# Kernel optimization log

Measured on AMD Instinct MI355X. Metric: run time of the kernel, lower is better.

Reference implementation:

```python
import jax, jax.numpy as jnp
import numpy as np

B, S, D, H = 1, 2048, 1024, 16
HD = D // H  # head_dim = 64
ROPE_BASE = 10000.0


def _rope_cos_sin(seqlen, head_dim, dtype):
    inv_freq = 1.0 / (ROPE_BASE ** (jnp.arange(0, head_dim, 2, dtype=jnp.float32) / head_dim))
    t = jnp.arange(seqlen, dtype=jnp.float32)
    freqs = jnp.outer(t, inv_freq)                      # [S, HD/2]
    emb = jnp.concatenate([freqs, freqs], axis=-1)      # [S, HD]
    # broadcast shape [1, S, 1, HD] over (batch, seq, heads, head_dim)
    return jnp.cos(emb)[None, :, None, :].astype(dtype), jnp.sin(emb)[None, :, None, :].astype(dtype)


def _rotate_half(x):
    x1, x2 = jnp.split(x, 2, axis=-1)
    return jnp.concatenate([-x2, x1], axis=-1)


def setup_inputs() -> dict:
    key = jax.random.key(0)
    k1, k2, k3 = jax.random.split(key, 3)
    std_in = 1.0 / np.sqrt(D)
    std_out = std_in / np.sqrt(2.0)  # layer_id = 0
    x = jax.random.normal(k1, (B, S, D), dtype=jnp.float32)
    w_in = jax.random.normal(k2, (3 * H * HD, D), dtype=jnp.float32) * std_in
    w_out = jax.random.normal(k3, (D, H * HD), dtype=jnp.float32) * std_out
    return {"x": x, "w_in": w_in, "w_out": w_out, "is_causal": 1}


def reference(x, w_in, w_out, is_causal):
    b, s, _ = x.shape
    qkv = jnp.einsum('bsd,ed->bse', x, w_in)            # [B,S,3*H*HD]
    xq, xk, xv = jnp.split(qkv, 3, axis=-1)
    xq = xq.reshape(b, s, H, HD)
    xk = xk.reshape(b, s, H, HD)
    xv = xv.reshape(b, s, H, HD)
    cos, sin = _rope_cos_sin(s, HD, xq.dtype)
    xq = xq * cos + _rotate_half(xq) * sin
    xk = xk * cos + _rotate_half(xk) * sin
    scale = 1.0 / np.sqrt(HD)
    scores = jnp.einsum('bqhd,bkhd->bhqk', xq, xk) * scale  # [B,H,S,S]
    if is_causal:
        mask = jnp.tril(jnp.ones((s, s), dtype=bool))
        scores = jnp.where(mask[None, None], scores, jnp.finfo(scores.dtype).min)
    probs = jax.nn.softmax(scores, axis=-1)
    out = jnp.einsum('bhqk,bkhd->bqhd', probs, xv)      # [B,S,H,HD]
    out = out.reshape(b, s, H * HD)
    return jnp.einsum('bse,de->bsd', out, w_out)
```

## Files before the change

### kernel.cpp

```cpp
#include <hip/hip_runtime.h>
#include <stdint.h>

#define S_LEN 2048
#define DMODEL 1024
#define NHEAD 16
#define HDIM 64
#define NE 3072
#define C2 0.18033688011112042f
#define RINV (-13.287712379549449f / 32.f)

typedef __attribute__((ext_vector_type(8))) short short8_t;
typedef __attribute__((ext_vector_type(4))) float f32x4;
typedef __attribute__((ext_vector_type(16))) float f32x16;

__device__ __forceinline__ float bf2f(ushort u) {
  union { float f; uint32_t i; } c; c.i = ((uint32_t)u) << 16; return c.f;
}
__device__ __forceinline__ ushort f2bf(float f) {
  union { float f; uint32_t i; } c; c.f = f;
  uint32_t x = c.i;
  return (ushort)((x + 0x7fffu + ((x >> 16) & 1u)) >> 16);
}

__device__ __forceinline__ void gload_lds16(const ushort* g, ushort* l) {
  __builtin_amdgcn_global_load_lds(
      (const __attribute__((address_space(1))) void*)g,
      (__attribute__((address_space(3))) void*)l, 16, 0, 0);
}

__global__ void cvt_all(const float* __restrict__ x, const float* __restrict__ w_in,
                        const float* __restrict__ w_out,
                        ushort* __restrict__ xbf, ushort* __restrict__ winbf,
                        ushort* __restrict__ woutbf) {
  int i = blockIdx.x * blockDim.x + threadIdx.x;
  const float* src; ushort* dst; int off;
  if (i < 524288)       { src = x;     dst = xbf;    off = i; }
  else if (i < 1310720) { src = w_in;  dst = winbf;  off = i - 524288; }
  else                  { src = w_out; dst = woutbf; off = i - 1310720; }
  float4 v = ((const float4*)src)[off];
  ushort4 o;
  o.x = f2bf(v.x); o.y = f2bf(v.y); o.z = f2bf(v.z); o.w = f2bf(v.w);
  ((ushort4*)dst)[off] = o;
}

template<int BM, int BN, int OUT_BF16>
__global__ __launch_bounds__(256) void gemm_abt(
    const ushort* __restrict__ A, const ushort* __restrict__ B,
    void* __restrict__ Cv, int M, int N, int K)
{
  constexpr int AR = BM / 32;
  constexpr int AC = BN / 32;
  constexpr int PG = (BM + BN) / 32;
  __shared__ ushort lds[(BM + BN) * 64];

  const int nbn = N / BN;
  const int cpx = gridDim.x >> 3;
  const int bid = blockIdx.x;
  const int swz = (bid & 7) * cpx + (bid >> 3);
  const int bm = swz / nbn;
  const int bn = swz - bm * nbn;
  const int tid = threadIdx.x;
  const int w = tid >> 6, l = tid & 63;
  const int wm = w >> 1, wn = w & 1;
  const int fr = l & 15, fg = l >> 4;

  f32x4 acc[AR][AC];
#pragma unroll
  for (int r = 0; r < AR; ++r)
#pragma unroll
    for (int c = 0; c < AC; ++c) acc[r][c] = (f32x4){0.f, 0.f, 0.f, 0.f};

  const ushort* gsrc[PG];
  ushort* ldst[PG];
#pragma unroll
  for (int i = 0; i < PG; ++i) {
    int ch = w + 4 * i;
    int row = ch * 8 + (l >> 3);
    if (row < BM)
      gsrc[i] = A + (size_t)(bm * BM + row) * K + (l & 7) * 8;
    else
      gsrc[i] = B + (size_t)(bn * BN + (row - BM)) * K + (l & 7) * 8;
    ldst[i] = &lds[ch * 512];
  }

  const ushort* fa = &lds[(wm * (BM / 2) + fr) * 64 + fg * 8];
  const ushort* fb = &lds[BM * 64 + (wn * (BN / 2) + fr) * 64 + fg * 8];

  for (int k0 = 0; k0 < K; k0 += 64) {
    __syncthreads();
#pragma unroll
    for (int i = 0; i < PG; ++i) gload_lds16(gsrc[i] + k0, ldst[i]);
    __syncthreads();

    short8_t af[AR][2], bfr[AC][2];
#pragma unroll
    for (int r = 0; r < AR; ++r)
#pragma unroll
      for (int kk = 0; kk < 2; ++kk) {
        union { short8_t v; uint4 q; } u;
        u.q = *(const uint4*)(fa + r * 1024 + kk * 32);
        af[r][kk] = u.v;
      }
#pragma unroll
    for (int c = 0; c < AC; ++c)
#pragma unroll
      for (int kk = 0; kk < 2; ++kk) {
        union { short8_t v; uint4 q; } u;
        u.q = *(const uint4*)(fb + c * 1024 + kk * 32);
        bfr[c][kk] = u.v;
      }
    __builtin_amdgcn_s_setprio(1);
#pragma unroll
    for (int kk = 0; kk < 2; ++kk)
#pragma unroll
      for (int r = 0; r < AR; ++r)
#pragma unroll
        for (int c = 0; c < AC; ++c)
          acc[r][c] = __builtin_amdgcn_mfma_f32_16x16x32_bf16(af[r][kk], bfr[c][kk], acc[r][c], 0, 0, 0);
    __builtin_amdgcn_s_setprio(0);
  }

  const int row0 = bm * BM + wm * (BM / 2) + fg * 4;
  const int col0 = bn * BN + wn * (BN / 2) + fr;
#pragma unroll
  for (int r = 0; r < AR; ++r)
#pragma unroll
    for (int c = 0; c < AC; ++c)
#pragma unroll
      for (int j = 0; j < 4; ++j) {
        int row = row0 + r * 16 + j;
        int col = col0 + c * 16;
        if (OUT_BF16)
          ((ushort*)Cv)[(size_t)row * N + col] = f2bf(acc[r][c][j]);
        else
          ((float*)Cv)[(size_t)row * N + col] = acc[r][c][j];
      }
}

__global__ __launch_bounds__(256) void transform_kv(
    const ushort* __restrict__ qkv, ushort* __restrict__ kfrag, ushort* __restrict__ vfrag)
{
  __shared__ ushort Kt[64][72];
  __shared__ ushort Vt[64][72];
  const int h = blockIdx.x & 15, t = blockIdx.x >> 4;
  const int tid = threadIdx.x;
#pragma unroll
  for (int it = 0; it < 2; ++it) {
    int idx = tid + 256 * it;
    int key = idx >> 3, d8 = (idx & 7) << 3;
    const ushort* src = qkv + (size_t)(t * 64 + key) * NE + DMODEL + h * HDIM + d8;
    *(uint4*)&Kt[key][d8] = *(const uint4*)src;
    *(uint4*)&Vt[key][d8] = *(const uint4*)(src + DMODEL);
  }
  __syncthreads();

  {
    const int i = tid & 31;
    const int k8 = (tid >> 5) * 8;
    float invf = exp2f((float)i * RINV);
#pragma unroll
    for (int kk = 0; kk < 8; ++kk) {
      int key = k8 + kk;
      float sn, cs;
      sincosf((float)(t * 64 + key) * invf, &sn, &cs);
      float x1 = bf2f(Kt[key][i]), x2 = bf2f(Kt[key][i + 32]);
      Kt[key][i]      = f2bf(x1 * cs - x2 * sn);
      Kt[key][i + 32] = f2bf(x2 * cs + x1 * sn);
    }
  }
  __syncthreads();

  ushort* kb = kfrag + (size_t)(h * 32 + t) * 4096;
  ushort* vb = vfrag + (size_t)(h * 32 + t) * 4096;
#pragma unroll
  for (int it = 0; it < 2; ++it) {
    int idx = tid + 256 * it;
    int c = idx >> 6, l = idx & 63;
    int q = l & 31, hi = l >> 5;
    int kh = c >> 2, ks = c & 3;
    uint4 v = *(const uint4*)&Kt[32 * kh + q][16 * ks + 8 * hi];
    *(uint4*)(kb + idx * 8) = v;
  }
#pragma unroll
  for (int it = 0; it < 2; ++it) {
    int idx = tid + 256 * it;
    int c = idx >> 6, l = idx & 63;
    int q = l & 31, hi = l >> 5;
    int ks = c >> 1, dh = c & 1;
    ushort tmp[8];
#pragma unroll
    for (int jj = 0; jj < 8; ++jj)
      tmp[jj] = Vt[16 * ks + 8 * hi + jj][32 * dh + q];
    *(uint4*)(vb + idx * 8) = *(const uint4*)tmp;
  }
}

__global__ __launch_bounds__(256) void attn_mfma(
    const ushort* __restrict__ qkv, const ushort* __restrict__ kfrag,
    const ushort* __restrict__ vfrag, ushort* __restrict__ O,
    const int* __restrict__ icausal)
{
  __shared__ ushort obf[4][32][68];
  __shared__ float2 mdl[4][32];

  const int h = blockIdx.x & 15;
  const int i = blockIdx.x >> 4;
  const int g = i & 15, k = i >> 4;
  const int qt = (k == 0) ? g : (k == 1) ? (63 - g) : (k == 2) ? (31 - g) : (32 + g);

  const int causal = *icausal;
  const int nt = causal ? ((qt >> 1) + 1) : (S_LEN / 64);

  const int tid = threadIdx.x;
  const int w = tid >> 6, l = tid & 63;
  const int q = l & 31, hi = l >> 5;
  const int q0 = qt * 32;
  const int qa = q0 + q;
  const int t0 = w * nt / 4, t1 = (w + 1) * nt / 4;

  short8_t qf[4];
  {
    const ushort* qp = qkv + (size_t)qa * NE + h * HDIM + 8 * hi;
#pragma unroll
    for (int ks = 0; ks < 4; ++ks) {
      union { short8_t v; uint4 u; } uu;
      uu.u = *(const uint4*)(qp + 16 * ks);
      qf[ks] = uu.v;
    }
    union { short8_t v; ushort u[8]; } a0, a1, b0, b1;
    a0.v = qf[0]; a1.v = qf[1]; b0.v = qf[2]; b1.v = qf[3];
#pragma unroll
    for (int j = 0; j < 8; ++j) {
      {
        float invf = exp2f((float)(8 * hi + j) * RINV);
        float sn, cs; sincosf((float)qa * invf, &sn, &cs);
        float x1 = bf2f(a0.u[j]), x2 = bf2f(b0.u[j]);
        a0.u[j] = f2bf(x1 * cs - x2 * sn);
        b0.u[j] = f2bf(x2 * cs + x1 * sn);
      }
      {
        float invf = exp2f((float)(16 + 8 * hi + j) * RINV);
        float sn, cs; sincosf((float)qa * invf, &sn, &cs);
        float x1 = bf2f(a1.u[j]), x2 = bf2f(b1.u[j]);
        a1.u[j] = f2bf(x1 * cs - x2 * sn);
        b1.u[j] = f2bf(x2 * cs + x1 * sn);
      }
    }
    qf[0] = a0.v; qf[1] = a1.v; qf[2] = b0.v; qf[3] = b1.v;
  }

  const ushort* kb = kfrag + (size_t)(h * 32 + t0) * 4096 + l * 8;
  const ushort* vb = vfrag + (size_t)(h * 32 + t0) * 4096 + l * 8;

  float m_run = -1e30f, den = 0.f;
  f32x16 oacc[2];
#pragma unroll
  for (int d = 0; d < 2; ++d)
#pragma unroll
    for (int r = 0; r < 16; ++r) oacc[d][r] = 0.f;

  if (t0 < t1) {
    uint4 kq[8];
#pragma unroll
    for (int ks = 0; ks < 4; ++ks)
#pragma unroll
      for (int kh = 0; kh < 2; ++kh)
        kq[ks * 2 + kh] = *(const uint4*)(kb + (kh * 4 + ks) * 512);
    kb += 4096;

    for (int t = t0; t < t1; ++t) {
      uint4 vq[8];
#pragma unroll
      for (int c = 0; c < 8; ++c)
        vq[c] = *(const uint4*)(vb + c * 512);
      vb += 4096;

      f32x16 sacc[2];
#pragma unroll
      for (int kh = 0; kh < 2; ++kh)
#pragma unroll
        for (int r = 0; r < 16; ++r) sacc[kh][r] = 0.f;
      __builtin_amdgcn_s_setprio(1);
#pragma unroll
      for (int ks = 0; ks < 4; ++ks)
#pragma unroll
        for (int kh = 0; kh < 2; ++kh) {
          union { short8_t v; uint4 u; } ku;
          ku.u = kq[ks * 2 + kh];
          sacc[kh] = __builtin_amdgcn_mfma_f32_32x32x16_bf16(ku.v, qf[ks], sacc[kh], 0, 0, 0);
        }
      __builtin_amdgcn_s_setprio(0);

      if (t + 1 < t1) {
#pragma unroll
        for (int ks = 0; ks < 4; ++ks)
#pragma unroll
          for (int kh = 0; kh < 2; ++kh)
            kq[ks * 2 + kh] = *(const uint4*)(kb + (kh * 4 + ks) * 512);
        kb += 4096;
      }

      if (causal && t == nt - 1) {
        const int k0 = t * 64;
#pragma unroll
        for (int kh = 0; kh < 2; ++kh)
#pragma unroll
          for (int r = 0; r < 16; ++r)
            if (k0 + 32 * kh + (r & 3) + 8 * (r >> 2) + 4 * hi > qa) sacc[kh][r] = -3e38f;
      }

      float v0 = -3e38f, v1 = -3e38f, v2 = -3e38f, v3 = -3e38f;
#pragma unroll
      for (int kh = 0; kh < 2; ++kh)
#pragma unroll
        for (int r = 0; r < 16; r += 4) {
          v0 = fmaxf(v0, sacc[kh][r + 0]);
          v1 = fmaxf(v1, sacc[kh][r + 1]);
          v2 = fmaxf(v2, sacc[kh][r + 2]);
          v3 = fmaxf(v3, sacc[kh][r + 3]);
        }
      float vmax = fmaxf(fmaxf(v0, v1), fmaxf(v2, v3));
      vmax = fmaxf(vmax, __shfl_xor(vmax, 32));

      if (__any(vmax > m_run + 44.3614196f)) {
        float mn = fmaxf(m_run, vmax);
        float alpha = exp2f((m_run - mn) * C2);
        den *= alpha;
#pragma unroll
        for (int d = 0; d < 2; ++d)
#pragma unroll
          for (int r = 0; r < 16; ++r) oacc[d][r] *= alpha;
        m_run = mn;
      }
      float mc2 = m_run * C2;
      float p0 = 0.f, p1 = 0.f, p2 = 0.f, p3 = 0.f;
#pragma unroll
      for (int kh = 0; kh < 2; ++kh)
#pragma unroll
        for (int r = 0; r < 16; r += 4) {
          float e0 = exp2f(fmaf(sacc[kh][r + 0], C2, -mc2));
          float e1 = exp2f(fmaf(sacc[kh][r + 1], C2, -mc2));
          float e2 = exp2f(fmaf(sacc[kh][r + 2], C2, -mc2));
          float e3 = exp2f(fmaf(sacc[kh][r + 3], C2, -mc2));
          sacc[kh][r + 0] = e0; sacc[kh][r + 1] = e1;
          sacc[kh][r + 2] = e2; sacc[kh][r + 3] = e3;
          p0 += e0; p1 += e1; p2 += e2; p3 += e3;
        }
      float psum = (p0 + p1) + (p2 + p3);
      psum += __shfl_xor(psum, 32);
      den += psum;

      short8_t pa[4];
#pragma unroll
      for (int ks = 0; ks < 4; ++ks) {
        const int blk = ks >> 1, kp = (ks & 1) * 8;
        uint wL0, wL1, wH0, wH1;
        asm("v_cvt_pk_bf16_f32 %0, %1, %2" : "=v"(wL0) : "v"(sacc[blk][kp + 0]), "v"(sacc[blk][kp + 1]));
        asm("v_cvt_pk_bf16_f32 %0, %1, %2" : "=v"(wL1) : "v"(sacc[blk][kp + 2]), "v"(sacc[blk][kp + 3]));
        asm("v_cvt_pk_bf16_f32 %0, %1, %2" : "=v"(wH0) : "v"(sacc[blk][kp + 4]), "v"(sacc[blk][kp + 5]));
        asm("v_cvt_pk_bf16_f32 %0, %1, %2" : "=v"(wH1) : "v"(sacc[blk][kp + 6]), "v"(sacc[blk][kp + 7]));
        uint s0 = hi ? wL0 : wH0, s1 = hi ? wL1 : wH1;
        uint r0 = __shfl_xor(s0, 32), r1 = __shfl_xor(s1, 32);
        union { short8_t v; uint u[4]; } pu;
        pu.u[0] = hi ? r0 : wL0;
        pu.u[1] = hi ? r1 : wL1;
        pu.u[2] = hi ? wH0 : r0;
        pu.u[3] = hi ? wH1 : r1;
        pa[ks] = pu.v;
      }

      __builtin_amdgcn_s_setprio(1);
#pragma unroll
      for (int ks = 0; ks < 4; ++ks)
#pragma unroll
        for (int dh = 0; dh < 2; ++dh) {
          union { short8_t v; uint4 u; } vu;
          vu.u = vq[ks * 2 + dh];
          oacc[dh] = __builtin_amdgcn_mfma_f32_32x32x16_bf16(vu.v, pa[ks], oacc[dh], 0, 0, 0);
        }
      __builtin_amdgcn_s_setprio(0);
    }
  }

#pragma unroll
  for (int dh = 0; dh < 2; ++dh)
#pragma unroll
    for (int rq = 0; rq < 4; ++rq) {
      uint a0, a1;
      asm("v_cvt_pk_bf16_f32 %0, %1, %2" : "=v"(a0) : "v"(oacc[dh][4 * rq + 0]), "v"(oacc[dh][4 * rq + 1]));
      asm("v_cvt_pk_bf16_f32 %0, %1, %2" : "=v"(a1) : "v"(oacc[dh][4 * rq + 2]), "v"(oacc[dh][4 * rq + 3]));
      uint2 dd; dd.x = a0; dd.y = a1;
      *(uint2*)&obf[w][q][32 * dh + 8 * rq + 4 * hi] = dd;
    }
  if (hi == 0) mdl[w][q] = make_float2(m_run, den);
  __syncthreads();

  {
    const int qq = tid >> 3, d8 = tid & 7;
    float2 md0 = mdl[0][qq], md1 = mdl[1][qq], md2 = mdl[2][qq], md3 = mdl[3][qq];
    float mt = fmaxf(fmaxf(md0.x, md1.x), fmaxf(md2.x, md3.x));
    float w0 = exp2f((md0.x - mt) * C2);
    float w1 = exp2f((md1.x - mt) * C2);
    float w2 = exp2f((md2.x - mt) * C2);
    float w3 = exp2f((md3.x - mt) * C2);
    float inv = 1.f / (md0.y * w0 + md1.y * w1 + md2.y * w2 + md3.y * w3);

    uint4 a = *(const uint4*)&obf[0][qq][d8 * 8];
    uint4 b = *(const uint4*)&obf[1][qq][d8 * 8];
    uint4 c = *(const uint4*)&obf[2][qq][d8 * 8];
    uint4 d = *(const uint4*)&obf[3][qq][d8 * 8];
    const ushort* ap = (const ushort*)&a;
    const ushort* bp = (const ushort*)&b;
    const ushort* cp = (const ushort*)&c;
    const ushort* dp = (const ushort*)&d;
    ushort out8[8];
#pragma unroll
    for (int e = 0; e < 8; ++e) {
      float acc = bf2f(ap[e]) * w0 + bf2f(bp[e]) * w1 + bf2f(cp[e]) * w2 + bf2f(dp[e]) * w3;
      out8[e] = f2bf(acc * inv);
    }
    *(uint4*)(O + (size_t)(q0 + qq) * DMODEL + h * HDIM + d8 * 8) = *(const uint4*)out8;
  }
}

extern "C" void kernel_launch(void* const* d_in, const int* in_sizes, int n_in,
                              void* d_out, int out_size, void* d_ws, size_t ws_size,
                              hipStream_t stream) {
  const float* x     = (const float*)d_in[0];
  const float* w_in  = (const float*)d_in[1];
  const float* w_out = (const float*)d_in[2];
  const int* icausal = (const int*)d_in[3];

  char* ws = (char*)d_ws;
  ushort* xbf    = (ushort*)(ws);
  ushort* winbf  = (ushort*)(ws + 4194304);
  ushort* woutbf = (ushort*)(ws + 10485760);
  ushort* qkv    = (ushort*)(ws + 12582912);
  ushort* obuf   = (ushort*)(ws + 25165824);
  ushort* vfrag  = xbf;
  ushort* kfrag  = winbf;

  cvt_all<<<6144, 256, 0, stream>>>(x, w_in, w_out, xbf, winbf, woutbf);

  gemm_abt<128, 64, 1><<<16 * 48, 256, 0, stream>>>(xbf, winbf, (void*)qkv, 2048, 3072, 1024);
  transform_kv<<<512, 256, 0, stream>>>(qkv, kfrag, vfrag);
  attn_mfma<<<1024, 256, 0, stream>>>(qkv, kfrag, vfrag, obuf, icausal);
  gemm_abt<64, 64, 0><<<32 * 16, 256, 0, stream>>>(obuf, woutbf, d_out, 2048, 1024, 1024);
}
```

Before: 85.94 us.

## Fuse K RoPE and K/V fragment repacking into QKV GEMM epilogue

Removes the separate transform_kv kernel. The QKV GEMM epilogue now writes Q to a compact buffer, stages the K and V tiles in LDS, applies RoPE to K, and writes the fragment-packed K/V layouts directly. This avoids one kernel launch and a full round trip of K/V through global memory. In exchange the GEMM epilogue gets longer, adds extra LDS syncs, and the K/V blocks do more work than the Q blocks.

```diff
diff --git a/kernel.cpp b/kernel.cpp
--- a/kernel.cpp
+++ b/kernel.cpp
@@ -43,10 +43,11 @@
   ((ushort4*)dst)[off] = o;
 }
 
-template<int BM, int BN, int OUT_BF16>
+template<int BM, int BN, int MODE>
 __global__ __launch_bounds__(256) void gemm_abt(
     const ushort* __restrict__ A, const ushort* __restrict__ B,
-    void* __restrict__ Cv, int M, int N, int K)
+    void* __restrict__ Cv, ushort* __restrict__ kfrag, ushort* __restrict__ vfrag,
+    int M, int N, int K)
 {
   constexpr int AR = BM / 32;
   constexpr int AC = BN / 32;
@@ -120,83 +121,87 @@
     __builtin_amdgcn_s_setprio(0);
   }
 
-  const int row0 = bm * BM + wm * (BM / 2) + fg * 4;
-  const int col0 = bn * BN + wn * (BN / 2) + fr;
-#pragma unroll
-  for (int r = 0; r < AR; ++r)
-#pragma unroll
-    for (int c = 0; c < AC; ++c)
-#pragma unroll
-      for (int j = 0; j < 4; ++j) {
-        int row = row0 + r * 16 + j;
-        int col = col0 + c * 16;
-        if (OUT_BF16)
-          ((ushort*)Cv)[(size_t)row * N + col] = f2bf(acc[r][c][j]);
-        else
-          ((float*)Cv)[(size_t)row * N + col] = acc[r][c][j];
-      }
-}
-
-__global__ __launch_bounds__(256) void transform_kv(
-    const ushort* __restrict__ qkv, ushort* __restrict__ kfrag, ushort* __restrict__ vfrag)
-{
-  __shared__ ushort Kt[64][72];
-  __shared__ ushort Vt[64][72];
-  const int h = blockIdx.x & 15, t = blockIdx.x >> 4;
-  const int tid = threadIdx.x;
-#pragma unroll
-  for (int it = 0; it < 2; ++it) {
-    int idx = tid + 256 * it;
-    int key = idx >> 3, d8 = (idx & 7) << 3;
-    const ushort* src = qkv + (size_t)(t * 64 + key) * NE + DMODEL + h * HDIM + d8;
-    *(uint4*)&Kt[key][d8] = *(const uint4*)src;
-    *(uint4*)&Vt[key][d8] = *(const uint4*)(src + DMODEL);
-  }
-  __syncthreads();
-
-  {
-    const int i = tid & 31;
-    const int k8 = (tid >> 5) * 8;
-    float invf = exp2f((float)i * RINV);
-#pragma unroll
-    for (int kk = 0; kk < 8; ++kk) {
-      int key = k8 + kk;
-      float sn, cs;
-      sincosf((float)(t * 64 + key) * invf, &sn, &cs);
-      float x1 = bf2f(Kt[key][i]), x2 = bf2f(Kt[key][i + 32]);
-      Kt[key][i]      = f2bf(x1 * cs - x2 * sn);
-      Kt[key][i + 32] = f2bf(x2 * cs + x1 * sn);
-    }
-  }
-  __syncthreads();
-
-  ushort* kb = kfrag + (size_t)(h * 32 + t) * 4096;
-  ushort* vb = vfrag + (size_t)(h * 32 + t) * 4096;
-#pragma unroll
-  for (int it = 0; it < 2; ++it) {
-    int idx = tid + 256 * it;
-    int c = idx >> 6, l = idx & 63;
-    int q = l & 31, hi = l >> 5;
-    int kh = c >> 2, ks = c & 3;
-    uint4 v = *(const uint4*)&Kt[32 * kh + q][16 * ks + 8 * hi];
-    *(uint4*)(kb + idx * 8) = v;
-  }
-#pragma unroll
-  for (int it = 0; it < 2; ++it) {
-    int idx = tid + 256 * it;
-    int c = idx >> 6, l = idx & 63;
-    int q = l & 31, hi = l >> 5;
-    int ks = c >> 1, dh = c & 1;
-    ushort tmp[8];
-#pragma unroll
-    for (int jj = 0; jj < 8; ++jj)
-      tmp[jj] = Vt[16 * ks + 8 * hi + jj][32 * dh + q];
-    *(uint4*)(vb + idx * 8) = *(const uint4*)tmp;
+  if constexpr (MODE == 0) {
+    const int row0 = bm * BM + wm * (BM / 2) + fg * 4;
+    const int col0 = bn * BN + wn * (BN / 2) + fr;
+#pragma unroll
+    for (int r = 0; r < AR; ++r)
+#pragma unroll
+      for (int c = 0; c < AC; ++c)
+#pragma unroll
+        for (int j = 0; j < 4; ++j)
+          ((float*)Cv)[(size_t)(row0 + r * 16 + j) * N + col0 + c * 16] = acc[r][c][j];
+  } else {
+    const int cls = bn >> 4;
+    const int h = bn & 15;
+    if (cls == 0) {
+      const int row0 = bm * BM + wm * (BM / 2) + fg * 4;
+      const int colq = bn * 64 + wn * 32 + fr;
+      ushort* qb = (ushort*)Cv;
+#pragma unroll
+      for (int r = 0; r < AR; ++r)
+#pragma unroll
+        for (int c = 0; c < AC; ++c)
+#pragma unroll
+          for (int j = 0; j < 4; ++j)
+            qb[(size_t)(row0 + r * 16 + j) * 1024 + colq + c * 16] = f2bf(acc[r][c][j]);
+    } else {
+      __syncthreads();
+      ushort* T = lds;
+#pragma unroll
+      for (int r = 0; r < AR; ++r)
+#pragma unroll
+        for (int c = 0; c < AC; ++c)
+#pragma unroll
+          for (int j = 0; j < 4; ++j) {
+            int rl = wm * 64 + r * 16 + fg * 4 + j;
+            int cl = wn * 32 + c * 16 + fr;
+            T[rl * 72 + cl] = f2bf(acc[r][c][j]);
+          }
+      __syncthreads();
+
+      if (cls == 1) {
+        const int ii = tid & 31;
+        const float invf = exp2f((float)ii * RINV);
+#pragma unroll
+        for (int kk = 0; kk < 16; ++kk) {
+          int key = (tid >> 5) * 16 + kk;
+          float sn, cs;
+          sincosf((float)(bm * 128 + key) * invf, &sn, &cs);
+          float x1 = bf2f(T[key * 72 + ii]), x2 = bf2f(T[key * 72 + ii + 32]);
+          T[key * 72 + ii]      = f2bf(x1 * cs - x2 * sn);
+          T[key * 72 + ii + 32] = f2bf(x2 * cs + x1 * sn);
+        }
+        __syncthreads();
+#pragma unroll
+        for (int it = 0; it < 4; ++it) {
+          int idx = tid + 256 * it;
+          int tt = idx >> 9, e = idx & 511;
+          int c2 = e >> 6, l2 = e & 63, q2 = l2 & 31, hi2 = l2 >> 5;
+          int kh = c2 >> 2, ks = c2 & 3;
+          uint4 v = *(const uint4*)&T[(64 * tt + 32 * kh + q2) * 72 + 16 * ks + 8 * hi2];
+          *(uint4*)(kfrag + (size_t)(h * 32 + bm * 2 + tt) * 4096 + e * 8) = v;
+        }
+      } else {
+#pragma unroll
+        for (int it = 0; it < 4; ++it) {
+          int idx = tid + 256 * it;
+          int tt = idx >> 9, e = idx & 511;
+          int c2 = e >> 6, l2 = e & 63, q2 = l2 & 31, hi2 = l2 >> 5;
+          int ks = c2 >> 1, dh = c2 & 1;
+          ushort tmp[8];
+#pragma unroll
+          for (int jj = 0; jj < 8; ++jj)
+            tmp[jj] = T[(64 * tt + 16 * ks + 8 * hi2 + jj) * 72 + 32 * dh + q2];
+          *(uint4*)(vfrag + (size_t)(h * 32 + bm * 2 + tt) * 4096 + e * 8) = *(const uint4*)tmp;
+        }
+      }
+    }
   }
 }
 
 __global__ __launch_bounds__(256) void attn_mfma(
-    const ushort* __restrict__ qkv, const ushort* __restrict__ kfrag,
+    const ushort* __restrict__ qbuf, const ushort* __restrict__ kfrag,
     const ushort* __restrict__ vfrag, ushort* __restrict__ O,
     const int* __restrict__ icausal)
 {
@@ -220,7 +225,7 @@
 
   short8_t qf[4];
   {
-    const ushort* qp = qkv + (size_t)qa * NE + h * HDIM + 8 * hi;
+    const ushort* qp = qbuf + (size_t)qa * 1024 + h * HDIM + 8 * hi;
 #pragma unroll
     for (int ks = 0; ks < 4; ++ks) {
       union { short8_t v; uint4 u; } uu;
@@ -435,15 +440,14 @@
   ushort* xbf    = (ushort*)(ws);
   ushort* winbf  = (ushort*)(ws + 4194304);
   ushort* woutbf = (ushort*)(ws + 10485760);
-  ushort* qkv    = (ushort*)(ws + 12582912);
+  ushort* qbuf   = (ushort*)(ws + 12582912);
+  ushort* kfrag  = (ushort*)(ws + 16777216);
+  ushort* vfrag  = (ushort*)(ws + 20971520);
   ushort* obuf   = (ushort*)(ws + 25165824);
-  ushort* vfrag  = xbf;
-  ushort* kfrag  = winbf;
 
   cvt_all<<<6144, 256, 0, stream>>>(x, w_in, w_out, xbf, winbf, woutbf);
 
-  gemm_abt<128, 64, 1><<<16 * 48, 256, 0, stream>>>(xbf, winbf, (void*)qkv, 2048, 3072, 1024);
-  transform_kv<<<512, 256, 0, stream>>>(qkv, kfrag, vfrag);
-  attn_mfma<<<1024, 256, 0, stream>>>(qkv, kfrag, vfrag, obuf, icausal);
-  gemm_abt<64, 64, 0><<<32 * 16, 256, 0, stream>>>(obuf, woutbf, d_out, 2048, 1024, 1024);
-}
+  gemm_abt<128, 64, 2><<<16 * 48, 256, 0, stream>>>(xbf, winbf, (void*)qbuf, kfrag, vfrag, 2048, 3072, 1024);
+  attn_mfma<<<1024, 256, 0, stream>>>(qbuf, kfrag, vfrag, obuf, icausal);
+  gemm_abt<64, 64, 0><<<32 * 16, 256, 0, stream>>>(obuf, woutbf, d_out, nullptr, nullptr, 2048, 1024, 1024);
+}
```

Result: faster. 81.23 us (-5.5%).
